# Performance work log

Measured on AMD Instinct MI355X. Metric: run time of the kernel, lower is better.

The kernel has to match this reference:

```python
import jax, jax.numpy as jnp
import numpy as np

N = 20000      # nodes
E = 160000     # edges (before self-loops)
B = 128        # graphs in batch
NEG_SLOPE = 0.2


def gat_layer(x, src, dst, W, a_src, a_dst, b):
    # x: [N, Cin]; W: [Cin, H*C]; a_src/a_dst: [H, C]; b: [C]
    H, C = a_src.shape
    n = x.shape[0]
    xw = (x @ W).reshape(n, H, C)                      # [N, H, C]
    alpha_src = jnp.sum(xw * a_src, axis=-1)           # [N, H]
    alpha_dst = jnp.sum(xw * a_dst, axis=-1)           # [N, H]
    e = jax.nn.leaky_relu(alpha_src[src] + alpha_dst[dst], NEG_SLOPE)  # [Etot, H]
    # numerically stable segment softmax over edges grouped by target node
    m = jax.ops.segment_max(e, dst, num_segments=n)    # [N, H]
    m = jnp.where(jnp.isfinite(m), m, 0.0)
    ex = jnp.exp(e - m[dst])                           # [Etot, H]
    den = jax.ops.segment_sum(ex, dst, num_segments=n) # [N, H]
    alpha = ex / (den[dst] + 1e-16)                    # [Etot, H]
    out = jax.ops.segment_sum(alpha[:, :, None] * xw[src], dst, num_segments=n)  # [N, H, C]
    return out.mean(axis=1) + b                        # concat=False -> head mean + bias


def setup_inputs() -> dict:
    key = jax.random.key(0)
    ks = jax.random.split(key, 12)
    s = 0.05
    x = jax.random.normal(ks[0], (N, 768), dtype=jnp.float32)
    edge_index = jax.random.randint(ks[1], (2, E), 0, N, dtype=jnp.int64)
    batch = jnp.sort(jax.random.randint(ks[2], (N,), 0, B, dtype=jnp.int64))
    W1 = jax.random.normal(ks[3], (768, 4 * 512), dtype=jnp.float32) * s
    a_src1 = jax.random.normal(ks[4], (4, 512), dtype=jnp.float32) * s
    a_dst1 = jax.random.normal(ks[5], (4, 512), dtype=jnp.float32) * s
    b1 = jnp.zeros((512,), dtype=jnp.float32)
    W2 = jax.random.normal(ks[6], (512, 4 * 256), dtype=jnp.float32) * s
    a_src2 = jax.random.normal(ks[7], (4, 256), dtype=jnp.float32) * s
    a_dst2 = jax.random.normal(ks[8], (4, 256), dtype=jnp.float32) * s
    b2 = jnp.zeros((256,), dtype=jnp.float32)
    fcW = jax.random.normal(ks[9], (256, 2), dtype=jnp.float32) * s
    fcb = jnp.zeros((2,), dtype=jnp.float32)
    return {"x": x, "edge_index": edge_index, "batch": batch,
            "W1": W1, "a_src1": a_src1, "a_dst1": a_dst1, "b1": b1,
            "W2": W2, "a_src2": a_src2, "a_dst2": a_dst2, "b2": b2,
            "fcW": fcW, "fcb": fcb}


def reference(x, edge_index, batch, W1, a_src1, a_dst1, b1, W2, a_src2, a_dst2, b2, fcW, fcb):
    n = x.shape[0]
    loops = jnp.arange(n, dtype=edge_index.dtype)      # GATConv adds self-loops by default
    src = jnp.concatenate([edge_index[0], loops])
    dst = jnp.concatenate([edge_index[1], loops])
    h = gat_layer(x, src, dst, W1, a_src1, a_dst1, b1)   # [N, 512]
    h = gat_layer(h, src, dst, W2, a_src2, a_dst2, b2)   # [N, 256]
    sums = jax.ops.segment_sum(h, batch, num_segments=B)                     # [B, 256]
    cnt = jax.ops.segment_sum(jnp.ones((n,), h.dtype), batch, num_segments=B)
    g = sums / jnp.maximum(cnt, 1.0)[:, None]            # scatter_mean
    return g @ fcW + fcb                                  # [B, 2]
```

## Files before the change

kernel.cpp:

```cpp
#include <hip/hip_runtime.h>

#define NN    20000
#define NE    160000
#define NETOT 180000
#define NB    128

typedef __attribute__((ext_vector_type(4))) float f32x4;
typedef __attribute__((ext_vector_type(8))) short s16x8;

__device__ __forceinline__ unsigned short f2bf(float f){
  unsigned u = __float_as_uint(f);
  return (unsigned short)((u + 0x7FFFu + ((u >> 16) & 1u)) >> 16);
}
__device__ __forceinline__ float bf2f(unsigned short h){
  return __uint_as_float(((unsigned)h) << 16);
}
__device__ __forceinline__ void gload16(const void* g, void* l){
  __builtin_amdgcn_global_load_lds((const __attribute__((address_space(1))) void*)g,
                                   (__attribute__((address_space(3))) void*)l, 16, 0, 0);
}

__global__ void k_cvt(const float* __restrict__ in, unsigned short* __restrict__ outp, int n4){
  int i = blockIdx.x * blockDim.x + threadIdx.x;
  if (i >= n4) return;
  float4 v = ((const float4*)in)[i];
  ushort4 h;
  h.x = f2bf(v.x); h.y = f2bf(v.y); h.z = f2bf(v.z); h.w = f2bf(v.w);
  ((ushort4*)outp)[i] = h;
}

__global__ void k_va(const float* __restrict__ W, const float* __restrict__ aS,
                     const float* __restrict__ aD, float* __restrict__ va, int K, int C){
  __shared__ float a_s[2048], a_d[2048];
  int t = threadIdx.x;
  int HC = 4 * C;
  for (int i = t; i < HC; i += 256){ a_s[i] = aS[i]; a_d[i] = aD[i]; }
  __syncthreads();
  int k = blockIdx.x * 4 + (t >> 6);
  int lane = t & 63;
  if (k >= K) return;
  float ss[4] = {0.f,0.f,0.f,0.f}, dd[4] = {0.f,0.f,0.f,0.f};
  for (int h = 0; h < 4; ++h)
    for (int c0 = 0; c0 < C; c0 += 64){
      float wv = W[(size_t)k * HC + h * C + c0 + lane];
      ss[h] += wv * a_s[h * C + c0 + lane];
      dd[h] += wv * a_d[h * C + c0 + lane];
    }
#pragma unroll
  for (int off = 32; off; off >>= 1)
#pragma unroll
    for (int h = 0; h < 4; ++h){
      ss[h] += __shfl_xor(ss[h], off);
      dd[h] += __shfl_xor(dd[h], off);
    }
  if (lane == 0)
#pragma unroll
    for (int h = 0; h < 4; ++h){
      va[h * K + k] = ss[h];
      va[(4 + h) * K + k] = dd[h];
    }
}

template<int K>
__global__ void k_alpha_in(const unsigned short* __restrict__ xf, const float* __restrict__ va,
                           float* __restrict__ asrc, float* __restrict__ adst){
  __shared__ float v_s[8 * K];
  int t = threadIdx.x;
  for (int i = t; i < 8 * K; i += 256) v_s[i] = va[i];
  __syncthreads();
  int n = blockIdx.x * 4 + (t >> 6);
  if (n >= NN) return;
  int lane = t & 63;
  const unsigned short* xr = xf + (size_t)n * K;
  float s[8] = {};
#pragma unroll
  for (int j = 0; j < K / 128; ++j){
    int idx = j * 128 + lane * 2;
    ushort2 xv = *(const ushort2*)(xr + idx);
    float f0 = bf2f(xv.x), f1 = bf2f(xv.y);
#pragma unroll
    for (int a = 0; a < 8; ++a)
      s[a] += f0 * v_s[a * K + idx] + f1 * v_s[a * K + idx + 1];
  }
#pragma unroll
  for (int off = 32; off; off >>= 1)
#pragma unroll
    for (int a = 0; a < 8; ++a) s[a] += __shfl_xor(s[a], off);
  if (lane == 0){
    ((float4*)asrc)[n] = make_float4(s[0], s[1], s[2], s[3]);
    ((float4*)adst)[n] = make_float4(s[4], s[5], s[6], s[7]);
  }
}

__global__ void k_count(const int* __restrict__ ei, int* __restrict__ counts){
  int e = blockIdx.x * blockDim.x + threadIdx.x;
  if (e >= NETOT) return;
  int d = (e < NE) ? ei[NE + e] : (e - NE);
  atomicAdd(&counts[d], 1);
}
__global__ void k_scan(const int* __restrict__ counts, int* __restrict__ row_ptr,
                       int* __restrict__ cursor){
  __shared__ int lds[1024];
  int t = threadIdx.x;
  int base = 0;
  for (int c0 = 0; c0 < NN; c0 += 1024){
    int i = c0 + t;
    int v = (i < NN) ? counts[i] : 0;
    __syncthreads();
    lds[t] = v;
    __syncthreads();
    for (int off = 1; off < 1024; off <<= 1){
      int x = (t >= off) ? lds[t - off] : 0;
      __syncthreads();
      lds[t] += x;
      __syncthreads();
    }
    int excl = base + lds[t] - v;
    if (i < NN){ row_ptr[i] = excl; cursor[i] = excl; }
    base += lds[1023];
  }
  if (t == 0) row_ptr[NN] = base;
}
__global__ void k_scatter(const int* __restrict__ ei, int* __restrict__ cursor,
                          int* __restrict__ csr_src){
  int e = blockIdx.x * blockDim.x + threadIdx.x;
  if (e >= NETOT) return;
  int s, d;
  if (e < NE){ s = ei[e]; d = ei[NE + e]; } else { s = d = e - NE; }
  int pos = atomicAdd(&cursor[d], 1);
  csr_src[pos] = s;
}

template<int K>
__global__ void k_aggx(const unsigned short* __restrict__ xf, const int* __restrict__ rp,
                       const int* __restrict__ csrc, const float* __restrict__ asrc,
                       const float* __restrict__ adst, unsigned short* __restrict__ agg){
  const int n = blockIdx.x, t = threadIdx.x;
  __shared__ float sm[4], srd[4];
  int beg = rp[n], end = rp[n + 1];
  float4 ad = ((const float4*)adst)[n];
  if (t < 64){
    float m0 = -1e30f, m1 = -1e30f, m2 = -1e30f, m3 = -1e30f;
    for (int i = beg + t; i < end; i += 64){
      int s = csrc[i];
      float4 as = ((const float4*)asrc)[s];
      float v0 = as.x + ad.x; v0 = v0 > 0.f ? v0 : 0.2f * v0; m0 = fmaxf(m0, v0);
      float v1 = as.y + ad.y; v1 = v1 > 0.f ? v1 : 0.2f * v1; m1 = fmaxf(m1, v1);
      float v2 = as.z + ad.z; v2 = v2 > 0.f ? v2 : 0.2f * v2; m2 = fmaxf(m2, v2);
      float v3 = as.w + ad.w; v3 = v3 > 0.f ? v3 : 0.2f * v3; m3 = fmaxf(m3, v3);
    }
#pragma unroll
    for (int off = 32; off; off >>= 1){
      m0 = fmaxf(m0, __shfl_xor(m0, off));
      m1 = fmaxf(m1, __shfl_xor(m1, off));
      m2 = fmaxf(m2, __shfl_xor(m2, off));
      m3 = fmaxf(m3, __shfl_xor(m3, off));
    }
    float s0 = 0.f, s1 = 0.f, s2 = 0.f, s3 = 0.f;
    for (int i = beg + t; i < end; i += 64){
      int s = csrc[i];
      float4 as = ((const float4*)asrc)[s];
      float v0 = as.x + ad.x; v0 = v0 > 0.f ? v0 : 0.2f * v0;
      float v1 = as.y + ad.y; v1 = v1 > 0.f ? v1 : 0.2f * v1;
      float v2 = as.z + ad.z; v2 = v2 > 0.f ? v2 : 0.2f * v2;
      float v3 = as.w + ad.w; v3 = v3 > 0.f ? v3 : 0.2f * v3;
      s0 += __expf(v0 - m0); s1 += __expf(v1 - m1);
      s2 += __expf(v2 - m2); s3 += __expf(v3 - m3);
    }
#pragma unroll
    for (int off = 32; off; off >>= 1){
      s0 += __shfl_xor(s0, off); s1 += __shfl_xor(s1, off);
      s2 += __shfl_xor(s2, off); s3 += __shfl_xor(s3, off);
    }
    if (t == 0){
      sm[0] = m0; sm[1] = m1; sm[2] = m2; sm[3] = m3;
      srd[0] = 1.f / (s0 + 1e-16f); srd[1] = 1.f / (s1 + 1e-16f);
      srd[2] = 1.f / (s2 + 1e-16f); srd[3] = 1.f / (s3 + 1e-16f);
    }
  }
  __syncthreads();
  float m0 = sm[0], m1 = sm[1], m2 = sm[2], m3 = sm[3];
  float r0 = srd[0], r1 = srd[1], r2 = srd[2], r3 = srd[3];
  float acc[4][4] = {};
  for (int i = beg; i < end; ++i){
    int s = csrc[i];
    float4 as = ((const float4*)asrc)[s];
    float v0 = as.x + ad.x; v0 = v0 > 0.f ? v0 : 0.2f * v0; float a0 = __expf(v0 - m0) * r0;
    float v1 = as.y + ad.y; v1 = v1 > 0.f ? v1 : 0.2f * v1; float a1 = __expf(v1 - m1) * r1;
    float v2 = as.z + ad.z; v2 = v2 > 0.f ? v2 : 0.2f * v2; float a2 = __expf(v2 - m2) * r2;
    float v3 = as.w + ad.w; v3 = v3 > 0.f ? v3 : 0.2f * v3; float a3 = __expf(v3 - m3) * r3;
    ushort4 xv = *(const ushort4*)(xf + (size_t)s * K + 4 * t);
    float f0 = bf2f(xv.x), f1 = bf2f(xv.y), f2 = bf2f(xv.z), f3 = bf2f(xv.w);
    acc[0][0] += a0 * f0; acc[0][1] += a0 * f1; acc[0][2] += a0 * f2; acc[0][3] += a0 * f3;
    acc[1][0] += a1 * f0; acc[1][1] += a1 * f1; acc[1][2] += a1 * f2; acc[1][3] += a1 * f3;
    acc[2][0] += a2 * f0; acc[2][1] += a2 * f1; acc[2][2] += a2 * f2; acc[2][3] += a2 * f3;
    acc[3][0] += a3 * f0; acc[3][1] += a3 * f1; acc[3][2] += a3 * f2; acc[3][3] += a3 * f3;
  }
#pragma unroll
  for (int h = 0; h < 4; ++h){
    ushort4 pk;
    pk.x = f2bf(acc[h][0]); pk.y = f2bf(acc[h][1]);
    pk.z = f2bf(acc[h][2]); pk.w = f2bf(acc[h][3]);
    *(ushort4*)(agg + (size_t)n * 4 * K + h * K + 4 * t) = pk;
  }
}

__global__ void k_tcvt_cat(const float* __restrict__ W, unsigned short* __restrict__ T,
                           int K, int C){
  __shared__ float tile[32][33];
  int tx = threadIdx.x, ty = threadIdx.y;
  int h = blockIdx.z;
  int c = blockIdx.x * 32 + tx, k = blockIdx.y * 32 + ty;
  tile[ty][tx] = W[(size_t)k * (4 * C) + h * C + c];
  __syncthreads();
  int c2 = blockIdx.x * 32 + ty, k2 = blockIdx.y * 32 + tx;
  T[(size_t)c2 * (4 * K) + h * K + k2] = f2bf(0.25f * tile[tx][ty]);
}

__global__ __launch_bounds__(256, 2)
void gemm_bf16(const unsigned short* __restrict__ A, const unsigned short* __restrict__ BT,
               const float* __restrict__ bias, unsigned short* __restrict__ C,
               int M, int N, int K, int ntile){
  __shared__ unsigned short lds[24576];
  const int t = threadIdx.x;
  const int lane = t & 63;
  const int w = t >> 6;
  const int wr = w >> 1, wc = w & 1;
  const int mt = blockIdx.x / ntile, nt = blockIdx.x % ntile;
  const int m0 = mt << 7, n0 = nt << 8;
  const int NK = K >> 5;

  int offA[4], offB[8];
#pragma unroll
  for (int mi = 0; mi < 4; ++mi){
    int row = wr * 64 + mi * 16 + (lane & 15);
    offA[mi] = row * 32 + (((lane >> 4) ^ ((row >> 1) & 3)) << 3);
  }
#pragma unroll
  for (int ni = 0; ni < 8; ++ni){
    int row = wc * 128 + ni * 16 + (lane & 15);
    offB[ni] = 4096 + row * 32 + (((lane >> 4) ^ ((row >> 1) & 3)) << 3);
  }

  const unsigned short* srcA[2]; int dstA[2];
#pragma unroll
  for (int j = 0; j < 2; ++j){
    int rA = w * 32 + j * 16 + (lane >> 2);
    int gr = m0 + rA; if (gr >= M) gr = M - 1;
    srcA[j] = A + (size_t)gr * K + (((lane & 3) ^ ((rA >> 1) & 3)) << 3);
    dstA[j] = w * 1024 + j * 512 + lane * 8;
  }
  const unsigned short* srcB[4]; int dstB[4];
#pragma unroll
  for (int j = 0; j < 4; ++j){
    int rB = w * 64 + j * 16 + (lane >> 2);
    srcB[j] = BT + (size_t)(n0 + rB) * K + (((lane & 3) ^ ((rB >> 1) & 3)) << 3);
    dstB[j] = 4096 + w * 2048 + j * 512 + lane * 8;
  }

#define STAGE(ks, bo) { int _k = (ks) << 5; \
    gload16(srcA[0] + _k, &lds[(bo) + dstA[0]]); \
    gload16(srcA[1] + _k, &lds[(bo) + dstA[1]]); \
    gload16(srcB[0] + _k, &lds[(bo) + dstB[0]]); \
    gload16(srcB[1] + _k, &lds[(bo) + dstB[1]]); \
    gload16(srcB[2] + _k, &lds[(bo) + dstB[2]]); \
    gload16(srcB[3] + _k, &lds[(bo) + dstB[3]]); }

  f32x4 acc[4][8];
#pragma unroll
  for (int i = 0; i < 4; ++i)
#pragma unroll
    for (int j = 0; j < 8; ++j) acc[i][j] = (f32x4){0.f, 0.f, 0.f, 0.f};

  STAGE(0, 0);
  asm volatile("s_waitcnt vmcnt(0)" ::: "memory");
  __builtin_amdgcn_sched_barrier(0);
  __builtin_amdgcn_s_barrier();
  __builtin_amdgcn_sched_barrier(0);

  for (int ks = 0; ks < NK; ++ks){
    const int bo = (ks & 1) * 12288;
    s16x8 av[4], bv[8];
#pragma unroll
    for (int i = 0; i < 4; ++i) av[i] = *(const s16x8*)&lds[bo + offA[i]];
#pragma unroll
    for (int i = 0; i < 8; ++i) bv[i] = *(const s16x8*)&lds[bo + offB[i]];
    if (ks + 1 < NK) STAGE(ks + 1, 12288 - bo);
    __builtin_amdgcn_s_setprio(1);
#pragma unroll
    for (int mi = 0; mi < 4; ++mi)
#pragma unroll
      for (int ni = 0; ni < 8; ++ni)
        acc[mi][ni] = __builtin_amdgcn_mfma_f32_16x16x32_bf16(av[mi], bv[ni], acc[mi][ni], 0, 0, 0);
    __builtin_amdgcn_s_setprio(0);
    asm volatile("s_waitcnt vmcnt(0)" ::: "memory");
    __builtin_amdgcn_sched_barrier(0);
    __builtin_amdgcn_s_barrier();
    __builtin_amdgcn_sched_barrier(0);
  }
#undef STAGE

  float bb[8];
#pragma unroll
  for (int ni = 0; ni < 8; ++ni)
    bb[ni] = bias[n0 + wc * 128 + ni * 16 + (lane & 15)];

#pragma unroll
  for (int h = 0; h < 2; ++h){
    if (wr == h){
#pragma unroll
      for (int mi = 0; mi < 4; ++mi)
#pragma unroll
        for (int ni = 0; ni < 8; ++ni)
#pragma unroll
          for (int r = 0; r < 4; ++r){
            int rl = mi * 16 + ((lane >> 4) << 2) + r;
            int col = wc * 128 + ni * 16 + (lane & 15);
            int byte = (rl * 512 + col * 2) ^ (((rl >> 2) & 3) << 5);
            *(unsigned short*)((char*)lds + byte) = f2bf(acc[mi][ni][r] + bb[ni]);
          }
    }
    __syncthreads();
#pragma unroll
    for (int it = 0; it < 8; ++it){
      int idx = it * 256 + t;
      int rl = idx >> 5, c16 = idx & 31;
      int byte = (rl * 512 + c16 * 16) ^ (((rl >> 2) & 3) << 5);
      s16x8 v = *(const s16x8*)((const char*)lds + byte);
      int grow = m0 + h * 64 + rl;
      if (grow < M)
        *(s16x8*)(C + (size_t)grow * N + n0 + c16 * 8) = v;
    }
    __syncthreads();
  }
}

__global__ void k_pool(const unsigned short* __restrict__ h2, const int* __restrict__ batch,
                       float* __restrict__ sums, int* __restrict__ cnt){
  int n0 = blockIdx.x * 64;
  int t = threadIdx.x;
  int nend = n0 + 64; if (nend > NN) nend = NN;
  int cur = batch[n0];
  float acc = 0.f; int run = 0;
  for (int n = n0; n < nend; ++n){
    int b = batch[n];
    if (b != cur){
      atomicAdd(&sums[cur * 256 + t], acc);
      if (t == 0) atomicAdd(&cnt[cur], run);
      acc = 0.f; run = 0; cur = b;
    }
    acc += bf2f(h2[(size_t)n * 256 + t]);
    run++;
  }
  atomicAdd(&sums[cur * 256 + t], acc);
  if (t == 0) atomicAdd(&cnt[cur], run);
}

__global__ void k_fc(const float* __restrict__ sums, const int* __restrict__ cnt,
                     const float* __restrict__ fcW, const float* __restrict__ fcb,
                     float* __restrict__ out){
  int b = blockIdx.x, t = threadIdx.x;
  int c = cnt[b]; if (c < 1) c = 1;
  float inv = 1.f / (float)c;
  float v = sums[b * 256 + t] * inv;
  float p0 = v * fcW[t * 2];
  float p1 = v * fcW[t * 2 + 1];
#pragma unroll
  for (int off = 32; off; off >>= 1){
    p0 += __shfl_xor(p0, off);
    p1 += __shfl_xor(p1, off);
  }
  __shared__ float r0[4], r1[4];
  if ((t & 63) == 0){ r0[t >> 6] = p0; r1[t >> 6] = p1; }
  __syncthreads();
  if (t == 0){
    out[b * 2 + 0] = r0[0] + r0[1] + r0[2] + r0[3] + fcb[0];
    out[b * 2 + 1] = r1[0] + r1[1] + r1[2] + r1[3] + fcb[1];
  }
}

extern "C" void kernel_launch(void* const* d_in, const int* in_sizes, int n_in,
                              void* d_out, int out_size, void* d_ws, size_t ws_size,
                              hipStream_t stream){
  const float* x      = (const float*)d_in[0];
  const int*   ei     = (const int*)d_in[1];
  const int*   batch  = (const int*)d_in[2];
  const float* W1     = (const float*)d_in[3];
  const float* a_src1 = (const float*)d_in[4];
  const float* a_dst1 = (const float*)d_in[5];
  const float* b1     = (const float*)d_in[6];
  const float* W2     = (const float*)d_in[7];
  const float* a_src2 = (const float*)d_in[8];
  const float* a_dst2 = (const float*)d_in[9];
  const float* b2     = (const float*)d_in[10];
  const float* fcW    = (const float*)d_in[11];
  const float* fcb    = (const float*)d_in[12];
  float* out = (float*)d_out;
  (void)in_sizes; (void)n_in; (void)out_size; (void)ws_size;

  char* ws = (char*)d_ws;
  size_t off = 0;
  auto take = [&](size_t bytes) -> char* {
    char* p = ws + off;
    off += (bytes + 255) & ~(size_t)255;
    return p;
  };
  char* slabA = take(122880000);
  unsigned short* agg1 = (unsigned short*)slabA;
  unsigned short* agg2 = (unsigned short*)slabA;
  char* slabB = take(30720000);
  unsigned short* x_bf  = (unsigned short*)slabB;
  unsigned short* h2_bf = (unsigned short*)slabB;
  unsigned short* h1_bf = (unsigned short*)take(20480000);
  unsigned short* Wc1T  = (unsigned short*)take(3145728);
  unsigned short* Wc2T  = (unsigned short*)take(1048576);
  float* va     = (float*)take(24576);
  float* asrc   = (float*)take(320000);
  float* adst   = (float*)take(320000);
  int* counts   = (int*)take(80004);
  int* row_ptr  = (int*)take(80004);
  int* cursor   = (int*)take(80004);
  int* csr_src  = (int*)take(720000);
  float* sums   = (float*)take(131072);
  int* cnt      = (int*)take(512);

  const int egrid = (NETOT + 255) / 256;

  hipMemsetAsync(counts, 0, NN * 4, stream);
  k_count<<<egrid, 256, 0, stream>>>(ei, counts);
  k_scan<<<1, 1024, 0, stream>>>(counts, row_ptr, cursor);
  k_scatter<<<egrid, 256, 0, stream>>>(ei, cursor, csr_src);

  k_cvt<<<(3840000 + 255) / 256, 256, 0, stream>>>(x, x_bf, 3840000);
  k_va<<<192, 256, 0, stream>>>(W1, a_src1, a_dst1, va, 768, 512);
  k_alpha_in<768><<<NN / 4, 256, 0, stream>>>(x_bf, va, asrc, adst);
  k_tcvt_cat<<<dim3(16, 24, 4), dim3(32, 32), 0, stream>>>(W1, Wc1T, 768, 512);
  k_aggx<768><<<NN, 192, 0, stream>>>(x_bf, row_ptr, csr_src, asrc, adst, agg1);
  gemm_bf16<<<157 * 2, 256, 0, stream>>>(agg1, Wc1T, b1, h1_bf, NN, 512, 3072, 2);

  k_va<<<128, 256, 0, stream>>>(W2, a_src2, a_dst2, va, 512, 256);
  k_alpha_in<512><<<NN / 4, 256, 0, stream>>>(h1_bf, va, asrc, adst);
  k_tcvt_cat<<<dim3(8, 16, 4), dim3(32, 32), 0, stream>>>(W2, Wc2T, 512, 256);
  k_aggx<512><<<NN, 128, 0, stream>>>(h1_bf, row_ptr, csr_src, asrc, adst, agg2);
  gemm_bf16<<<157 * 1, 256, 0, stream>>>(agg2, Wc2T, b2, h2_bf, NN, 256, 2048, 1);

  hipMemsetAsync(sums, 0, 131072, stream);
  hipMemsetAsync(cnt, 0, 512, stream);
  k_pool<<<(NN + 63) / 64, 256, 0, stream>>>(h2_bf, batch, sums, cnt);
  k_fc<<<NB, 256, 0, stream>>>(sums, cnt, fcW, fcb, out);
}
```

Before: 518.0 us.

## Precompute edge softmax, triple-buffer GEMM loads, warp-shuffle scan, widen alpha loads

Adds a separate edge kernel that computes normalized attention coefficients once per edge and stores them. The aggregation kernels then read these instead of redoing max, exp and sum in every block. The GEMM moves from double to triple buffering of LDS stages with finer vmcnt waits, trading more LDS for deeper prefetch. The scan now uses a wave-shuffle scan and also zeroes the pooling buffers, which removes two memsets. The alpha_in loop reads four elements per lane. Costs are an extra edge-sized buffer write and read, more LDS per GEMM block, and an extra barrier per k-step.

```diff
diff --git a/kernel.cpp b/kernel.cpp
--- a/kernel.cpp
+++ b/kernel.cpp
@@ -74,13 +74,15 @@
   const unsigned short* xr = xf + (size_t)n * K;
   float s[8] = {};
 #pragma unroll
-  for (int j = 0; j < K / 128; ++j){
-    int idx = j * 128 + lane * 2;
-    ushort2 xv = *(const ushort2*)(xr + idx);
-    float f0 = bf2f(xv.x), f1 = bf2f(xv.y);
-#pragma unroll
-    for (int a = 0; a < 8; ++a)
-      s[a] += f0 * v_s[a * K + idx] + f1 * v_s[a * K + idx + 1];
+  for (int j = 0; j < K / 256; ++j){
+    int idx = j * 256 + lane * 4;
+    ushort4 xv = *(const ushort4*)(xr + idx);
+    float f0 = bf2f(xv.x), f1 = bf2f(xv.y), f2 = bf2f(xv.z), f3 = bf2f(xv.w);
+#pragma unroll
+    for (int a = 0; a < 8; ++a){
+      const float* vp = v_s + a * K + idx;
+      s[a] += f0 * vp[0] + f1 * vp[1] + f2 * vp[2] + f3 * vp[3];
+    }
   }
 #pragma unroll
   for (int off = 32; off; off >>= 1)
@@ -99,25 +101,39 @@
   atomicAdd(&counts[d], 1);
 }
 __global__ void k_scan(const int* __restrict__ counts, int* __restrict__ row_ptr,
-                       int* __restrict__ cursor){
-  __shared__ int lds[1024];
+                       int* __restrict__ cursor, float* __restrict__ sums,
+                       int* __restrict__ cnt){
   int t = threadIdx.x;
+  for (int i = t; i < NB * 256; i += 1024) sums[i] = 0.f;
+  if (t < NB) cnt[t] = 0;
+  __shared__ int wsum[16];
+  int wid = t >> 6, lane = t & 63;
   int base = 0;
   for (int c0 = 0; c0 < NN; c0 += 1024){
     int i = c0 + t;
     int v = (i < NN) ? counts[i] : 0;
+    int s = v;
+#pragma unroll
+    for (int off = 1; off < 64; off <<= 1){
+      int u = __shfl_up(s, off);
+      if (lane >= off) s += u;
+    }
+    if (lane == 63) wsum[wid] = s;
     __syncthreads();
-    lds[t] = v;
+    if (wid == 0){
+      int ws = (lane < 16) ? wsum[lane] : 0;
+#pragma unroll
+      for (int off = 1; off < 16; off <<= 1){
+        int u = __shfl_up(ws, off);
+        if (lane >= off) ws += u;
+      }
+      if (lane < 16) wsum[lane] = ws;
+    }
     __syncthreads();
-    for (int off = 1; off < 1024; off <<= 1){
-      int x = (t >= off) ? lds[t - off] : 0;
-      __syncthreads();
-      lds[t] += x;
-      __syncthreads();
-    }
-    int excl = base + lds[t] - v;
+    int excl = base + (wid ? wsum[wid - 1] : 0) + s - v;
     if (i < NN){ row_ptr[i] = excl; cursor[i] = excl; }
-    base += lds[1023];
+    base += wsum[15];
+    __syncthreads();
   }
   if (t == 0) row_ptr[NN] = base;
 }
@@ -131,70 +147,72 @@
   csr_src[pos] = s;
 }
 
+__global__ void k_edge(const int* __restrict__ rp, const int* __restrict__ csrc,
+                       const float* __restrict__ asrc, const float* __restrict__ adst,
+                       float* __restrict__ alpha4){
+  int n = blockIdx.x * 4 + (threadIdx.x >> 6);
+  if (n >= NN) return;
+  int lane = threadIdx.x & 63;
+  int beg = rp[n], end = rp[n + 1];
+  float4 ad = ((const float4*)adst)[n];
+  float mx0 = -1e30f, mx1 = -1e30f, mx2 = -1e30f, mx3 = -1e30f;
+  for (int i = beg + lane; i < end; i += 64){
+    int s = csrc[i];
+    float4 as = ((const float4*)asrc)[s];
+    float v0 = as.x + ad.x; v0 = v0 > 0.f ? v0 : 0.2f * v0; mx0 = fmaxf(mx0, v0);
+    float v1 = as.y + ad.y; v1 = v1 > 0.f ? v1 : 0.2f * v1; mx1 = fmaxf(mx1, v1);
+    float v2 = as.z + ad.z; v2 = v2 > 0.f ? v2 : 0.2f * v2; mx2 = fmaxf(mx2, v2);
+    float v3 = as.w + ad.w; v3 = v3 > 0.f ? v3 : 0.2f * v3; mx3 = fmaxf(mx3, v3);
+  }
+#pragma unroll
+  for (int off = 32; off; off >>= 1){
+    mx0 = fmaxf(mx0, __shfl_xor(mx0, off));
+    mx1 = fmaxf(mx1, __shfl_xor(mx1, off));
+    mx2 = fmaxf(mx2, __shfl_xor(mx2, off));
+    mx3 = fmaxf(mx3, __shfl_xor(mx3, off));
+  }
+  float s0 = 0.f, s1 = 0.f, s2 = 0.f, s3 = 0.f;
+  for (int i = beg + lane; i < end; i += 64){
+    int s = csrc[i];
+    float4 as = ((const float4*)asrc)[s];
+    float v0 = as.x + ad.x; v0 = v0 > 0.f ? v0 : 0.2f * v0;
+    float v1 = as.y + ad.y; v1 = v1 > 0.f ? v1 : 0.2f * v1;
+    float v2 = as.z + ad.z; v2 = v2 > 0.f ? v2 : 0.2f * v2;
+    float v3 = as.w + ad.w; v3 = v3 > 0.f ? v3 : 0.2f * v3;
+    float e0 = __expf(v0 - mx0), e1 = __expf(v1 - mx1);
+    float e2 = __expf(v2 - mx2), e3 = __expf(v3 - mx3);
+    s0 += e0; s1 += e1; s2 += e2; s3 += e3;
+    ((float4*)alpha4)[i] = make_float4(e0, e1, e2, e3);
+  }
+#pragma unroll
+  for (int off = 32; off; off >>= 1){
+    s0 += __shfl_xor(s0, off); s1 += __shfl_xor(s1, off);
+    s2 += __shfl_xor(s2, off); s3 += __shfl_xor(s3, off);
+  }
+  float r0 = 1.f / (s0 + 1e-16f), r1 = 1.f / (s1 + 1e-16f);
+  float r2 = 1.f / (s2 + 1e-16f), r3 = 1.f / (s3 + 1e-16f);
+  for (int i = beg + lane; i < end; i += 64){
+    float4 v = ((const float4*)alpha4)[i];
+    ((float4*)alpha4)[i] = make_float4(v.x * r0, v.y * r1, v.z * r2, v.w * r3);
+  }
+}
+
 template<int K>
 __global__ void k_aggx(const unsigned short* __restrict__ xf, const int* __restrict__ rp,
-                       const int* __restrict__ csrc, const float* __restrict__ asrc,
-                       const float* __restrict__ adst, unsigned short* __restrict__ agg){
+                       const int* __restrict__ csrc, const float* __restrict__ alpha4,
+                       unsigned short* __restrict__ agg){
   const int n = blockIdx.x, t = threadIdx.x;
-  __shared__ float sm[4], srd[4];
   int beg = rp[n], end = rp[n + 1];
-  float4 ad = ((const float4*)adst)[n];
-  if (t < 64){
-    float m0 = -1e30f, m1 = -1e30f, m2 = -1e30f, m3 = -1e30f;
-    for (int i = beg + t; i < end; i += 64){
-      int s = csrc[i];
-      float4 as = ((const float4*)asrc)[s];
-      float v0 = as.x + ad.x; v0 = v0 > 0.f ? v0 : 0.2f * v0; m0 = fmaxf(m0, v0);
-      float v1 = as.y + ad.y; v1 = v1 > 0.f ? v1 : 0.2f * v1; m1 = fmaxf(m1, v1);
-      float v2 = as.z + ad.z; v2 = v2 > 0.f ? v2 : 0.2f * v2; m2 = fmaxf(m2, v2);
-      float v3 = as.w + ad.w; v3 = v3 > 0.f ? v3 : 0.2f * v3; m3 = fmaxf(m3, v3);
-    }
-#pragma unroll
-    for (int off = 32; off; off >>= 1){
-      m0 = fmaxf(m0, __shfl_xor(m0, off));
-      m1 = fmaxf(m1, __shfl_xor(m1, off));
-      m2 = fmaxf(m2, __shfl_xor(m2, off));
-      m3 = fmaxf(m3, __shfl_xor(m3, off));
-    }
-    float s0 = 0.f, s1 = 0.f, s2 = 0.f, s3 = 0.f;
-    for (int i = beg + t; i < end; i += 64){
-      int s = csrc[i];
-      float4 as = ((const float4*)asrc)[s];
-      float v0 = as.x + ad.x; v0 = v0 > 0.f ? v0 : 0.2f * v0;
-      float v1 = as.y + ad.y; v1 = v1 > 0.f ? v1 : 0.2f * v1;
-      float v2 = as.z + ad.z; v2 = v2 > 0.f ? v2 : 0.2f * v2;
-      float v3 = as.w + ad.w; v3 = v3 > 0.f ? v3 : 0.2f * v3;
-      s0 += __expf(v0 - m0); s1 += __expf(v1 - m1);
-      s2 += __expf(v2 - m2); s3 += __expf(v3 - m3);
-    }
-#pragma unroll
-    for (int off = 32; off; off >>= 1){
-      s0 += __shfl_xor(s0, off); s1 += __shfl_xor(s1, off);
-      s2 += __shfl_xor(s2, off); s3 += __shfl_xor(s3, off);
-    }
-    if (t == 0){
-      sm[0] = m0; sm[1] = m1; sm[2] = m2; sm[3] = m3;
-      srd[0] = 1.f / (s0 + 1e-16f); srd[1] = 1.f / (s1 + 1e-16f);
-      srd[2] = 1.f / (s2 + 1e-16f); srd[3] = 1.f / (s3 + 1e-16f);
-    }
-  }
-  __syncthreads();
-  float m0 = sm[0], m1 = sm[1], m2 = sm[2], m3 = sm[3];
-  float r0 = srd[0], r1 = srd[1], r2 = srd[2], r3 = srd[3];
   float acc[4][4] = {};
   for (int i = beg; i < end; ++i){
     int s = csrc[i];
-    float4 as = ((const float4*)asrc)[s];
-    float v0 = as.x + ad.x; v0 = v0 > 0.f ? v0 : 0.2f * v0; float a0 = __expf(v0 - m0) * r0;
-    float v1 = as.y + ad.y; v1 = v1 > 0.f ? v1 : 0.2f * v1; float a1 = __expf(v1 - m1) * r1;
-    float v2 = as.z + ad.z; v2 = v2 > 0.f ? v2 : 0.2f * v2; float a2 = __expf(v2 - m2) * r2;
-    float v3 = as.w + ad.w; v3 = v3 > 0.f ? v3 : 0.2f * v3; float a3 = __expf(v3 - m3) * r3;
+    float4 al = ((const float4*)alpha4)[i];
     ushort4 xv = *(const ushort4*)(xf + (size_t)s * K + 4 * t);
     float f0 = bf2f(xv.x), f1 = bf2f(xv.y), f2 = bf2f(xv.z), f3 = bf2f(xv.w);
-    acc[0][0] += a0 * f0; acc[0][1] += a0 * f1; acc[0][2] += a0 * f2; acc[0][3] += a0 * f3;
-    acc[1][0] += a1 * f0; acc[1][1] += a1 * f1; acc[1][2] += a1 * f2; acc[1][3] += a1 * f3;
-    acc[2][0] += a2 * f0; acc[2][1] += a2 * f1; acc[2][2] += a2 * f2; acc[2][3] += a2 * f3;
-    acc[3][0] += a3 * f0; acc[3][1] += a3 * f1; acc[3][2] += a3 * f2; acc[3][3] += a3 * f3;
+    acc[0][0] += al.x * f0; acc[0][1] += al.x * f1; acc[0][2] += al.x * f2; acc[0][3] += al.x * f3;
+    acc[1][0] += al.y * f0; acc[1][1] += al.y * f1; acc[1][2] += al.y * f2; acc[1][3] += al.y * f3;
+    acc[2][0] += al.z * f0; acc[2][1] += al.z * f1; acc[2][2] += al.z * f2; acc[2][3] += al.z * f3;
+    acc[3][0] += al.w * f0; acc[3][1] += al.w * f1; acc[3][2] += al.w * f2; acc[3][3] += al.w * f3;
   }
 #pragma unroll
   for (int h = 0; h < 4; ++h){
@@ -221,7 +239,7 @@
 void gemm_bf16(const unsigned short* __restrict__ A, const unsigned short* __restrict__ BT,
                const float* __restrict__ bias, unsigned short* __restrict__ C,
                int M, int N, int K, int ntile){
-  __shared__ unsigned short lds[24576];
+  __shared__ unsigned short lds[36864];
   const int t = threadIdx.x;
   const int lane = t & 63;
   const int w = t >> 6;
@@ -258,13 +276,13 @@
     dstB[j] = 4096 + w * 2048 + j * 512 + lane * 8;
   }
 
-#define STAGE(ks, bo) { int _k = (ks) << 5; \
-    gload16(srcA[0] + _k, &lds[(bo) + dstA[0]]); \
-    gload16(srcA[1] + _k, &lds[(bo) + dstA[1]]); \
-    gload16(srcB[0] + _k, &lds[(bo) + dstB[0]]); \
-    gload16(srcB[1] + _k, &lds[(bo) + dstB[1]]); \
-    gload16(srcB[2] + _k, &lds[(bo) + dstB[2]]); \
-    gload16(srcB[3] + _k, &lds[(bo) + dstB[3]]); }
+#define STAGE(ks, bo_) { int _k = (ks) << 5; \
+    gload16(srcA[0] + _k, &lds[(bo_) + dstA[0]]); \
+    gload16(srcA[1] + _k, &lds[(bo_) + dstA[1]]); \
+    gload16(srcB[0] + _k, &lds[(bo_) + dstB[0]]); \
+    gload16(srcB[1] + _k, &lds[(bo_) + dstB[1]]); \
+    gload16(srcB[2] + _k, &lds[(bo_) + dstB[2]]); \
+    gload16(srcB[3] + _k, &lds[(bo_) + dstB[3]]); }
 
   f32x4 acc[4][8];
 #pragma unroll
@@ -272,20 +290,28 @@
 #pragma unroll
     for (int j = 0; j < 8; ++j) acc[i][j] = (f32x4){0.f, 0.f, 0.f, 0.f};
 
-  STAGE(0, 0);
-  asm volatile("s_waitcnt vmcnt(0)" ::: "memory");
-  __builtin_amdgcn_sched_barrier(0);
-  __builtin_amdgcn_s_barrier();
-  __builtin_amdgcn_sched_barrier(0);
-
+  STAGE(0, 0); STAGE(1, 12288); STAGE(2, 24576);
+
+  int bo = 0;
   for (int ks = 0; ks < NK; ++ks){
-    const int bo = (ks & 1) * 12288;
+    if (ks < NK - 2)      { asm volatile("s_waitcnt vmcnt(12)" ::: "memory"); }
+    else if (ks == NK - 2){ asm volatile("s_waitcnt vmcnt(6)" ::: "memory"); }
+    else                  { asm volatile("s_waitcnt vmcnt(0)" ::: "memory"); }
+    __builtin_amdgcn_sched_barrier(0);
+    __builtin_amdgcn_s_barrier();
+    __builtin_amdgcn_sched_barrier(0);
+
     s16x8 av[4], bv[8];
 #pragma unroll
     for (int i = 0; i < 4; ++i) av[i] = *(const s16x8*)&lds[bo + offA[i]];
 #pragma unroll
     for (int i = 0; i < 8; ++i) bv[i] = *(const s16x8*)&lds[bo + offB[i]];
-    if (ks + 1 < NK) STAGE(ks + 1, 12288 - bo);
+    asm volatile("s_waitcnt lgkmcnt(0)" ::: "memory");
+    __builtin_amdgcn_sched_barrier(0);
+    __builtin_amdgcn_s_barrier();
+    __builtin_amdgcn_sched_barrier(0);
+    if (ks + 3 < NK) STAGE(ks + 3, bo);
+
     __builtin_amdgcn_s_setprio(1);
 #pragma unroll
     for (int mi = 0; mi < 4; ++mi)
@@ -293,10 +319,7 @@
       for (int ni = 0; ni < 8; ++ni)
         acc[mi][ni] = __builtin_amdgcn_mfma_f32_16x16x32_bf16(av[mi], bv[ni], acc[mi][ni], 0, 0, 0);
     __builtin_amdgcn_s_setprio(0);
-    asm volatile("s_waitcnt vmcnt(0)" ::: "memory");
-    __builtin_amdgcn_sched_barrier(0);
-    __builtin_amdgcn_s_barrier();
-    __builtin_amdgcn_sched_barrier(0);
+    bo += 12288; if (bo == 36864) bo = 0;
   }
 #undef STAGE
 
@@ -305,6 +328,7 @@
   for (int ni = 0; ni < 8; ++ni)
     bb[ni] = bias[n0 + wc * 128 + ni * 16 + (lane & 15)];
 
+  __builtin_amdgcn_s_barrier();
 #pragma unroll
   for (int h = 0; h < 2; ++h){
     if (wr == h){
@@ -417,6 +441,7 @@
   float* va     = (float*)take(24576);
   float* asrc   = (float*)take(320000);
   float* adst   = (float*)take(320000);
+  float* alpha4 = (float*)take((size_t)NETOT * 16);
   int* counts   = (int*)take(80004);
   int* row_ptr  = (int*)take(80004);
   int* cursor   = (int*)take(80004);
@@ -428,24 +453,24 @@
 
   hipMemsetAsync(counts, 0, NN * 4, stream);
   k_count<<<egrid, 256, 0, stream>>>(ei, counts);
-  k_scan<<<1, 1024, 0, stream>>>(counts, row_ptr, cursor);
+  k_scan<<<1, 1024, 0, stream>>>(counts, row_ptr, cursor, sums, cnt);
   k_scatter<<<egrid, 256, 0, stream>>>(ei, cursor, csr_src);
 
   k_cvt<<<(3840000 + 255) / 256, 256, 0, stream>>>(x, x_bf, 3840000);
   k_va<<<192, 256, 0, stream>>>(W1, a_src1, a_dst1, va, 768, 512);
   k_alpha_in<768><<<NN / 4, 256, 0, stream>>>(x_bf, va, asrc, adst);
   k_tcvt_cat<<<dim3(16, 24, 4), dim3(32, 32), 0, stream>>>(W1, Wc1T, 768, 512);
-  k_aggx<768><<<NN, 192, 0, stream>>>(x_bf, row_ptr, csr_src, asrc, adst, agg1);
+  k_edge<<<(NN + 3) / 4, 256, 0, stream>>>(row_ptr, csr_src, asrc, adst, alpha4);
+  k_aggx<768><<<NN, 192, 0, stream>>>(x_bf, row_ptr, csr_src, alpha4, agg1);
   gemm_bf16<<<157 * 2, 256, 0, stream>>>(agg1, Wc1T, b1, h1_bf, NN, 512, 3072, 2);
 
   k_va<<<128, 256, 0, stream>>>(W2, a_src2, a_dst2, va, 512, 256);
   k_alpha_in<512><<<NN / 4, 256, 0, stream>>>(h1_bf, va, asrc, adst);
   k_tcvt_cat<<<dim3(8, 16, 4), dim3(32, 32), 0, stream>>>(W2, Wc2T, 512, 256);
-  k_aggx<512><<<NN, 128, 0, stream>>>(h1_bf, row_ptr, csr_src, asrc, adst, agg2);
-  gemm_bf16<<<157 * 1, 256, 0, stream>>>(agg2, Wc2T, b2, h2_bf, NN, 256, 2048, 1);
-
-  hipMemsetAsync(sums, 0, 131072, stream);
-  hipMemsetAsync(cnt, 0, 512, stream);
+  k_edge<<<(NN + 3) / 4, 256, 0, stream>>>(row_ptr, csr_src, asrc, adst, alpha4);
+  k_aggx<512><<<NN, 128, 0, stream>>>(h1_bf, row_ptr, csr_src, alpha4, agg2);
+  gemm_bf16<<<157, 256, 0, stream>>>(agg2, Wc2T, b2, h2_bf, NN, 256, 2048, 1);
+
   k_pool<<<(NN + 63) / 64, 256, 0, stream>>>(h2_bf, batch, sums, cnt);
   k_fc<<<NB, 256, 0, stream>>>(sums, cnt, fcW, fcb, out);
 }
```

Result: no change. 510.4 us (-1.5%).
